# Kernel optimization log

Hardware: AMD Instinct MI355X
Metric: run time of the kernel (lower is better)

## Reference

```python
import jax, jax.numpy as jnp
import numpy as np

N, F_IN, F_OUT = 8192, 256, 256
ALPHA = 0.2  # LeakyReLU negative slope
NEG = -9e15

def setup_inputs() -> dict:
    key = jax.random.key(0)
    k1, k2, k3, k4, k5 = jax.random.split(key, 5)
    h = jax.random.normal(k1, (N, F_IN), dtype=jnp.float32)
    adj = jax.random.randint(k2, (N, N), 0, 2, dtype=jnp.int32)
    W_w = jax.random.normal(k3, (F_IN, F_OUT), dtype=jnp.float32) / np.sqrt(F_IN)
    W_b = jax.random.normal(k4, (F_OUT,), dtype=jnp.float32) * 0.01
    a = jax.random.normal(k5, (2 * F_OUT, 1), dtype=jnp.float32) / np.sqrt(2 * F_OUT)
    return {"h": h, "adj": adj, "W_w": W_w, "W_b": W_b, "a": a}

def reference(h, adj, W_w, W_b, a):
    # Wh: [N, F_OUT]
    Wh = h @ W_w + W_b
    a1 = a[:F_OUT, 0]   # scores for source node i (row)
    a2 = a[F_OUT:, 0]   # scores for target node j (col)
    # e[i,j] = leakyrelu(Wh_i . a1 + Wh_j . a2)  -- separable form of the
    # original repeat/cat construction, identical math without the NxNx2F tensor.
    e = jax.nn.leaky_relu((Wh @ a1)[:, None] + (Wh @ a2)[None, :], negative_slope=ALPHA)
    attention = jnp.where(adj > 0, e, NEG)
    attention = jax.nn.softmax(attention, axis=1)
    # dropout is identity in eval / p=0
    h_prime = attention @ Wh  # [N, F_OUT]
    return h_prime
```

## Files before the change

### kernel.cpp

```cpp
#include <hip/hip_runtime.h>
#include <stdint.h>

#define NN 8192
#define FD 256
#define LOG2E 1.44269504088896340736f
#define SPLIT 8
#define JSLICE (NN / SPLIT)
#define NIT (JSLICE / 32)

typedef __attribute__((ext_vector_type(8))) __bf16 bf16x8;
typedef __attribute__((ext_vector_type(4))) float f32x4;

__device__ __forceinline__ unsigned short f2bf(float x) {
    unsigned u = __float_as_uint(x);
    u = u + 0x7fffu + ((u >> 16) & 1u);
    return (unsigned short)(u >> 16);
}
__device__ __forceinline__ bf16x8 ld_bf8(const unsigned short* p) {
    uint4 v = *(const uint4*)p;
    return __builtin_bit_cast(bf16x8, v);
}
__device__ __forceinline__ unsigned pack_trunc2(float a, float b) {
    return __builtin_amdgcn_perm(__float_as_uint(b), __float_as_uint(a), 0x07060302u);
}
__device__ __forceinline__ void async_ld16(const void* g, void* lds) {
    __builtin_amdgcn_global_load_lds(
        (const __attribute__((address_space(1))) void*)g,
        (__attribute__((address_space(3))) void*)lds, 16, 0, 0);
}

__global__ __launch_bounds__(256) void wtrans_kernel(const float* __restrict__ W,
                                                     unsigned short* __restrict__ WbT) {
    int idx = blockIdx.x * 256 + threadIdx.x;
    int k = idx >> 8, f = idx & 255;
    WbT[f * 256 + k] = f2bf(W[idx]);
}

__global__ __launch_bounds__(256) void gemm1_kernel(const float* __restrict__ h,
                                                    const unsigned short* __restrict__ WbT,
                                                    const float* __restrict__ bias,
                                                    const float* __restrict__ av,
                                                    unsigned short* __restrict__ PBu,
                                                    float* __restrict__ f1p,
                                                    float* __restrict__ f2p) {
    __shared__ float Wh_s[256 * 33];
    __shared__ float red_s[2 * 8 * 32];
    int t = threadIdx.x;
    int l = t & 63, w = t >> 6;
    int jc = (blockIdx.x & 7) * 32 + (blockIdx.x >> 3);
    int i0 = jc * 32;
    int fbase = w * 64;
    int cl = l & 15, q = l >> 4;

    f32x4 acc[2][4] = {};
    const float* hA0 = h + (size_t)(i0 + cl) * FD;
    const float* hA1 = h + (size_t)(i0 + 16 + cl) * FD;

    #pragma unroll
    for (int ks = 0; ks < 8; ++ks) {
        int kk = ks * 32 + q * 8;
        union { unsigned short u[8]; bf16x8 v; } ua0, ua1;
        float4 x0 = *(const float4*)(hA0 + kk);
        float4 x1 = *(const float4*)(hA0 + kk + 4);
        float4 y0 = *(const float4*)(hA1 + kk);
        float4 y1 = *(const float4*)(hA1 + kk + 4);
        ua0.u[0]=f2bf(x0.x); ua0.u[1]=f2bf(x0.y); ua0.u[2]=f2bf(x0.z); ua0.u[3]=f2bf(x0.w);
        ua0.u[4]=f2bf(x1.x); ua0.u[5]=f2bf(x1.y); ua0.u[6]=f2bf(x1.z); ua0.u[7]=f2bf(x1.w);
        ua1.u[0]=f2bf(y0.x); ua1.u[1]=f2bf(y0.y); ua1.u[2]=f2bf(y0.z); ua1.u[3]=f2bf(y0.w);
        ua1.u[4]=f2bf(y1.x); ua1.u[5]=f2bf(y1.y); ua1.u[6]=f2bf(y1.z); ua1.u[7]=f2bf(y1.w);
        #pragma unroll
        for (int bg = 0; bg < 4; ++bg) {
            bf16x8 bF = ld_bf8(WbT + (fbase + bg * 16 + cl) * 256 + kk);
            acc[0][bg] = __builtin_amdgcn_mfma_f32_16x16x32_bf16(ua0.v, bF, acc[0][bg], 0, 0, 0);
            acc[1][bg] = __builtin_amdgcn_mfma_f32_16x16x32_bf16(ua1.v, bF, acc[1][bg], 0, 0, 0);
        }
    }

    #pragma unroll
    for (int mt = 0; mt < 2; ++mt)
        #pragma unroll
        for (int bg = 0; bg < 4; ++bg)
            #pragma unroll
            for (int e = 0; e < 4; ++e) {
                int il = mt * 16 + q * 4 + e;
                int fl = fbase + bg * 16 + cl;
                Wh_s[fl * 33 + il] = acc[mt][bg][e] + bias[fl];
            }
    __syncthreads();
    {
        size_t jcBase = (size_t)jc * 8192;
        #pragma unroll
        for (int u = 0; u < 4; ++u) {
            int fg = u * 4 + (t >> 6);
            int ll = t & 63;
            int c2 = ll & 15, q2 = ll >> 4;
            const float* src = &Wh_s[(fg * 16 + c2) * 33 + q2 * 8];
            union { unsigned short us[8]; uint4 v; } p;
            #pragma unroll
            for (int e = 0; e < 8; ++e) p.us[e] = f2bf(src[e]);
            *(uint4*)(PBu + jcBase + fg * 512 + ll * 8) = p.v;
        }
    }
    {
        int i = t & 31, fc = t >> 5;
        float s1 = 0.f, s2 = 0.f;
        #pragma unroll
        for (int fo = 0; fo < 32; ++fo) {
            int f = fc * 32 + fo;
            float wv = Wh_s[f * 33 + i];
            s1 += wv * av[f];
            s2 += wv * av[256 + f];
        }
        red_s[fc * 32 + i] = s1;
        red_s[256 + fc * 32 + i] = s2;
    }
    __syncthreads();
    if (t < 32) {
        float s = 0.f;
        #pragma unroll
        for (int fc = 0; fc < 8; ++fc) s += red_s[fc * 32 + t];
        f1p[i0 + t] = s * LOG2E;
    } else if (t < 64) {
        int i = t - 32;
        float s = 0.f;
        #pragma unroll
        for (int fc = 0; fc < 8; ++fc) s += red_s[256 + fc * 32 + i];
        f2p[i0 + i] = s * LOG2E;
    }
}

__global__ __launch_bounds__(256, 4) void gat_kernel(const int* __restrict__ adj,
                                                     const unsigned short* __restrict__ PBu,
                                                     const float* __restrict__ f1p,
                                                     const float* __restrict__ f2p,
                                                     float* __restrict__ num,
                                                     float* __restrict__ den) {
    __shared__ __align__(16) unsigned short Bs[2][8192];
    __shared__ unsigned mask_b[2][64];
    __shared__ float f2_s[JSLICE];

    int t = threadIdx.x;
    int l = t & 63, w = t >> 6;
    int s = blockIdx.x & 7;
    int strip = blockIdx.x >> 3;
    int i0b = strip * 64;
    int j0 = s * JSLICE;
    int jw0 = j0 / 32;
    int cl = l & 15, q = l >> 4;

    *(float4*)&f2_s[t * 4] = *(const float4*)(f2p + j0 + t * 4);

    const char* pbBase = (const char*)(PBu + (size_t)jw0 * 8192);
    #pragma unroll
    for (int k = 0; k < 4; ++k)
        async_ld16(pbBase + k * 4096 + t * 16, (char*)&Bs[0][0] + k * 4096 + t * 16);

    const int* arow = adj + (size_t)(i0b + w * 16 + (l >> 5)) * NN + j0 + (l & 31);
    {
        int v0 = arow[0 * 2 * NN], v1 = arow[1 * 2 * NN], v2 = arow[2 * 2 * NN], v3 = arow[3 * 2 * NN];
        int v4 = arow[4 * 2 * NN], v5 = arow[5 * 2 * NN], v6 = arow[6 * 2 * NN], v7 = arow[7 * 2 * NN];
        unsigned long long b0 = __ballot(v0 > 0), b1 = __ballot(v1 > 0);
        unsigned long long b2 = __ballot(v2 > 0), b3 = __ballot(v3 > 0);
        unsigned long long b4 = __ballot(v4 > 0), b5 = __ballot(v5 > 0);
        unsigned long long b6 = __ballot(v6 > 0), b7 = __ballot(v7 > 0);
        if (l == 0) {
            *(uint2*)&mask_b[0][w * 16 + 0]  = make_uint2((unsigned)b0, (unsigned)(b0 >> 32));
            *(uint2*)&mask_b[0][w * 16 + 2]  = make_uint2((unsigned)b1, (unsigned)(b1 >> 32));
            *(uint2*)&mask_b[0][w * 16 + 4]  = make_uint2((unsigned)b2, (unsigned)(b2 >> 32));
            *(uint2*)&mask_b[0][w * 16 + 6]  = make_uint2((unsigned)b3, (unsigned)(b3 >> 32));
            *(uint2*)&mask_b[0][w * 16 + 8]  = make_uint2((unsigned)b4, (unsigned)(b4 >> 32));
            *(uint2*)&mask_b[0][w * 16 + 10] = make_uint2((unsigned)b5, (unsigned)(b5 >> 32));
            *(uint2*)&mask_b[0][w * 16 + 12] = make_uint2((unsigned)b6, (unsigned)(b6 >> 32));
            *(uint2*)&mask_b[0][w * 16 + 14] = make_uint2((unsigned)b7, (unsigned)(b7 >> 32));
        }
    }

    float f1v = f1p[i0b + w * 16 + cl];

    const bf16x8 onesB = __builtin_bit_cast(bf16x8,
        make_uint4(0x3F803F80u, 0x3F803F80u, 0x3F803F80u, 0x3F803F80u));

    f32x4 acc[16] = {};
    f32x4 accR = {};

    #pragma unroll 1
    for (int g = 0; g < NIT; ++g) {
        __syncthreads();
        int a0, a1, a2, a3, a4, a5, a6, a7;
        if (g + 1 < NIT) {
            const char* src = pbBase + (size_t)(g + 1) * 16384;
            char* dst = (char*)&Bs[(g + 1) & 1][0];
            #pragma unroll
            for (int k = 0; k < 4; ++k)
                async_ld16(src + k * 4096 + t * 16, dst + k * 4096 + t * 16);
            int jo = (g + 1) * 32;
            a0 = arow[0 * 2 * NN + jo]; a1 = arow[1 * 2 * NN + jo];
            a2 = arow[2 * 2 * NN + jo]; a3 = arow[3 * 2 * NN + jo];
            a4 = arow[4 * 2 * NN + jo]; a5 = arow[5 * 2 * NN + jo];
            a6 = arow[6 * 2 * NN + jo]; a7 = arow[7 * 2 * NN + jo];
        }

        unsigned mw = mask_b[g & 1][w * 16 + cl];
        float4 F0 = *(const float4*)&f2_s[g * 32 + q * 8];
        float4 F1 = *(const float4*)&f2_s[g * 32 + q * 8 + 4];

        unsigned bits = mw >> (q * 8);
        float fe[8] = {F0.x, F0.y, F0.z, F0.w, F1.x, F1.y, F1.z, F1.w};
        float wv[8];
        #pragma unroll
        for (int e = 0; e < 8; ++e) {
            float sv = f1v + fe[e];
            sv = fmaxf(sv, 0.2f * sv);
            float x = __builtin_amdgcn_exp2f(sv);
            x = (bits >> e) & 1 ? x : 0.f;
            wv[e] = x;
        }
        union { unsigned uu[4]; bf16x8 v; } af;
        af.uu[0] = pack_trunc2(wv[0], wv[1]);
        af.uu[1] = pack_trunc2(wv[2], wv[3]);
        af.uu[2] = pack_trunc2(wv[4], wv[5]);
        af.uu[3] = pack_trunc2(wv[6], wv[7]);

        const unsigned short* bu = &Bs[g & 1][0] + l * 8;
        #pragma unroll
        for (int fg = 0; fg < 16; ++fg) {
            bf16x8 B = ld_bf8(bu + fg * 512);
            acc[fg] = __builtin_amdgcn_mfma_f32_16x16x32_bf16(af.v, B, acc[fg], 0, 0, 0);
        }
        accR = __builtin_amdgcn_mfma_f32_16x16x32_bf16(af.v, onesB, accR, 0, 0, 0);

        if (g + 1 < NIT) {
            int nb = (g + 1) & 1;
            unsigned long long b0 = __ballot(a0 > 0), b1 = __ballot(a1 > 0);
            unsigned long long b2 = __ballot(a2 > 0), b3 = __ballot(a3 > 0);
            unsigned long long b4 = __ballot(a4 > 0), b5 = __ballot(a5 > 0);
            unsigned long long b6 = __ballot(a6 > 0), b7 = __ballot(a7 > 0);
            if (l == 0) {
                *(uint2*)&mask_b[nb][w * 16 + 0]  = make_uint2((unsigned)b0, (unsigned)(b0 >> 32));
                *(uint2*)&mask_b[nb][w * 16 + 2]  = make_uint2((unsigned)b1, (unsigned)(b1 >> 32));
                *(uint2*)&mask_b[nb][w * 16 + 4]  = make_uint2((unsigned)b2, (unsigned)(b2 >> 32));
                *(uint2*)&mask_b[nb][w * 16 + 6]  = make_uint2((unsigned)b3, (unsigned)(b3 >> 32));
                *(uint2*)&mask_b[nb][w * 16 + 8]  = make_uint2((unsigned)b4, (unsigned)(b4 >> 32));
                *(uint2*)&mask_b[nb][w * 16 + 10] = make_uint2((unsigned)b5, (unsigned)(b5 >> 32));
                *(uint2*)&mask_b[nb][w * 16 + 12] = make_uint2((unsigned)b6, (unsigned)(b6 >> 32));
                *(uint2*)&mask_b[nb][w * 16 + 14] = make_uint2((unsigned)b7, (unsigned)(b7 >> 32));
            }
        }
    }

    if (cl == 0) {
        #pragma unroll
        for (int e = 0; e < 4; ++e)
            den[(size_t)s * NN + i0b + w * 16 + q * 4 + e] = accR[e];
    }

    float* nrow = num + (size_t)s * NN * FD;
    #pragma unroll
    for (int e = 0; e < 4; ++e) {
        int r = i0b + w * 16 + q * 4 + e;
        #pragma unroll
        for (int fg = 0; fg < 16; ++fg)
            nrow[(size_t)r * FD + fg * 16 + cl] = acc[fg][e];
    }
}

__global__ __launch_bounds__(256) void combine_kernel(const float* __restrict__ num,
                                                      const float* __restrict__ den,
                                                      float* __restrict__ out) {
    int idx = blockIdx.x * 256 + threadIdx.x;
    int i = idx >> 8;
    float nsum = 0.f, dsum = 0.f;
    #pragma unroll
    for (int s = 0; s < SPLIT; ++s) {
        nsum += num[(size_t)s * NN * FD + idx];
        dsum += den[(size_t)s * NN + i];
    }
    out[idx] = nsum / dsum;
}

extern "C" void kernel_launch(void* const* d_in, const int* in_sizes, int n_in,
                              void* d_out, int out_size, void* d_ws, size_t ws_size,
                              hipStream_t stream) {
    const float* h   = (const float*)d_in[0];
    const int*   adj = (const int*)d_in[1];
    const float* W   = (const float*)d_in[2];
    const float* b   = (const float*)d_in[3];
    const float* a   = (const float*)d_in[4];
    float* out = (float*)d_out;

    char* ws = (char*)d_ws;
    unsigned short* PBu = (unsigned short*)ws;
    unsigned short* WbT = (unsigned short*)(ws + (4u << 20));
    float* f1p = (float*)(ws + (4u << 20) + (128u << 10));
    float* f2p = f1p + NN;
    float* den = f2p + NN;
    float* num = (float*)(ws + (24u << 20));

    wtrans_kernel<<<256, 256, 0, stream>>>(W, WbT);
    gemm1_kernel<<<256, 256, 0, stream>>>(h, WbT, b, a, PBu, f1p, f2p);
    gat_kernel<<<128 * SPLIT, 256, 0, stream>>>(adj, PBu, f1p, f2p, num, den);
    combine_kernel<<<NN * FD / 256, 256, 0, stream>>>(num, den, out);
}
```

Before: 436.1 us.

## Load adjacency as int4 over 64-column chunks with shuffle-built masks

The adjacency read switches from scalar 32-column loads per iteration to 16-byte vector loads covering 64 columns every two iterations. The per-row bitmasks are now built with xor-shuffle OR reductions instead of ballots, and written into a four-slot mask ring. The goal is fewer, wider global load instructions on the dominant adj stream, which is 256 MB of int32, and looser coupling between loads and compute. In exchange the code adds shuffle work, an extra barrier, and more complex slot indexing, which could introduce race or ordering errors.

```diff
diff --git a/kernel.cpp b/kernel.cpp
--- a/kernel.cpp
+++ b/kernel.cpp
@@ -7,6 +7,7 @@
 #define SPLIT 8
 #define JSLICE (NN / SPLIT)
 #define NIT (JSLICE / 32)
+#define NADJ (JSLICE / 64)
 
 typedef __attribute__((ext_vector_type(8))) __bf16 bf16x8;
 typedef __attribute__((ext_vector_type(4))) float f32x4;
@@ -136,7 +137,7 @@
                                                      float* __restrict__ num,
                                                      float* __restrict__ den) {
     __shared__ __align__(16) unsigned short Bs[2][8192];
-    __shared__ unsigned mask_b[2][64];
+    __shared__ unsigned mask_b[4][64];
     __shared__ float f2_s[JSLICE];
 
     int t = threadIdx.x;
@@ -155,27 +156,33 @@
     for (int k = 0; k < 4; ++k)
         async_ld16(pbBase + k * 4096 + t * 16, (char*)&Bs[0][0] + k * 4096 + t * 16);
 
-    const int* arow = adj + (size_t)(i0b + w * 16 + (l >> 5)) * NN + j0 + (l & 31);
+    const int* abase = adj + (size_t)(i0b + w * 16 + (l >> 4)) * NN + j0 + (l & 15) * 4;
+    int4 A0 = *(const int4*)(abase + 0 * 4 * NN);
+    int4 A1 = *(const int4*)(abase + 1 * 4 * NN);
+    int4 A2 = *(const int4*)(abase + 2 * 4 * NN);
+    int4 A3 = *(const int4*)(abase + 3 * 4 * NN);
+
+    float f1v = f1p[i0b + w * 16 + cl];
+
+    __syncthreads();
+
     {
-        int v0 = arow[0 * 2 * NN], v1 = arow[1 * 2 * NN], v2 = arow[2 * 2 * NN], v3 = arow[3 * 2 * NN];
-        int v4 = arow[4 * 2 * NN], v5 = arow[5 * 2 * NN], v6 = arow[6 * 2 * NN], v7 = arow[7 * 2 * NN];
-        unsigned long long b0 = __ballot(v0 > 0), b1 = __ballot(v1 > 0);
-        unsigned long long b2 = __ballot(v2 > 0), b3 = __ballot(v3 > 0);
-        unsigned long long b4 = __ballot(v4 > 0), b5 = __ballot(v5 > 0);
-        unsigned long long b6 = __ballot(v6 > 0), b7 = __ballot(v7 > 0);
-        if (l == 0) {
-            *(uint2*)&mask_b[0][w * 16 + 0]  = make_uint2((unsigned)b0, (unsigned)(b0 >> 32));
-            *(uint2*)&mask_b[0][w * 16 + 2]  = make_uint2((unsigned)b1, (unsigned)(b1 >> 32));
-            *(uint2*)&mask_b[0][w * 16 + 4]  = make_uint2((unsigned)b2, (unsigned)(b2 >> 32));
-            *(uint2*)&mask_b[0][w * 16 + 6]  = make_uint2((unsigned)b3, (unsigned)(b3 >> 32));
-            *(uint2*)&mask_b[0][w * 16 + 8]  = make_uint2((unsigned)b4, (unsigned)(b4 >> 32));
-            *(uint2*)&mask_b[0][w * 16 + 10] = make_uint2((unsigned)b5, (unsigned)(b5 >> 32));
-            *(uint2*)&mask_b[0][w * 16 + 12] = make_uint2((unsigned)b6, (unsigned)(b6 >> 32));
-            *(uint2*)&mask_b[0][w * 16 + 14] = make_uint2((unsigned)b7, (unsigned)(b7 >> 32));
-        }
-    }
-
-    float f1v = f1p[i0b + w * 16 + cl];
+        int word = (l >> 3) & 1;
+        int sh = 4 * (l & 7);
+        int rsub = l >> 4;
+        #pragma unroll
+        for (int ld = 0; ld < 4; ++ld) {
+            int4 A = ld == 0 ? A0 : ld == 1 ? A1 : ld == 2 ? A2 : A3;
+            unsigned n = (unsigned)(A.x > 0) | ((unsigned)(A.y > 0) << 1)
+                       | ((unsigned)(A.z > 0) << 2) | ((unsigned)(A.w > 0) << 3);
+            unsigned v = n << sh;
+            v |= __shfl_xor(v, 1);
+            v |= __shfl_xor(v, 2);
+            v |= __shfl_xor(v, 4);
+            if ((l & 7) == 0)
+                mask_b[word][w * 16 + ld * 4 + rsub] = v;
+        }
+    }
 
     const bf16x8 onesB = __builtin_bit_cast(bf16x8,
         make_uint4(0x3F803F80u, 0x3F803F80u, 0x3F803F80u, 0x3F803F80u));
@@ -186,21 +193,47 @@
     #pragma unroll 1
     for (int g = 0; g < NIT; ++g) {
         __syncthreads();
-        int a0, a1, a2, a3, a4, a5, a6, a7;
+
         if (g + 1 < NIT) {
             const char* src = pbBase + (size_t)(g + 1) * 16384;
             char* dst = (char*)&Bs[(g + 1) & 1][0];
             #pragma unroll
             for (int k = 0; k < 4; ++k)
                 async_ld16(src + k * 4096 + t * 16, dst + k * 4096 + t * 16);
-            int jo = (g + 1) * 32;
-            a0 = arow[0 * 2 * NN + jo]; a1 = arow[1 * 2 * NN + jo];
-            a2 = arow[2 * 2 * NN + jo]; a3 = arow[3 * 2 * NN + jo];
-            a4 = arow[4 * 2 * NN + jo]; a5 = arow[5 * 2 * NN + jo];
-            a6 = arow[6 * 2 * NN + jo]; a7 = arow[7 * 2 * NN + jo];
-        }
-
-        unsigned mw = mask_b[g & 1][w * 16 + cl];
+        }
+
+        if ((g & 1) == 0) {
+            int c1 = g / 2 + 1;
+            if (c1 < NADJ) {
+                int jo = c1 * 64;
+                A0 = *(const int4*)(abase + 0 * 4 * NN + jo);
+                A1 = *(const int4*)(abase + 1 * 4 * NN + jo);
+                A2 = *(const int4*)(abase + 2 * 4 * NN + jo);
+                A3 = *(const int4*)(abase + 3 * 4 * NN + jo);
+            }
+        } else {
+            int c1 = (g + 1) / 2;
+            if (c1 < NADJ) {
+                int word = (l >> 3) & 1;
+                int slot = (g + 1 + word) & 3;
+                int sh = 4 * (l & 7);
+                int rsub = l >> 4;
+                #pragma unroll
+                for (int ld = 0; ld < 4; ++ld) {
+                    int4 A = ld == 0 ? A0 : ld == 1 ? A1 : ld == 2 ? A2 : A3;
+                    unsigned n = (unsigned)(A.x > 0) | ((unsigned)(A.y > 0) << 1)
+                               | ((unsigned)(A.z > 0) << 2) | ((unsigned)(A.w > 0) << 3);
+                    unsigned v = n << sh;
+                    v |= __shfl_xor(v, 1);
+                    v |= __shfl_xor(v, 2);
+                    v |= __shfl_xor(v, 4);
+                    if ((l & 7) == 0)
+                        mask_b[slot][w * 16 + ld * 4 + rsub] = v;
+                }
+            }
+        }
+
+        unsigned mw = mask_b[g & 3][w * 16 + cl];
         float4 F0 = *(const float4*)&f2_s[g * 32 + q * 8];
         float4 F1 = *(const float4*)&f2_s[g * 32 + q * 8 + 4];
 
@@ -228,24 +261,6 @@
             acc[fg] = __builtin_amdgcn_mfma_f32_16x16x32_bf16(af.v, B, acc[fg], 0, 0, 0);
         }
         accR = __builtin_amdgcn_mfma_f32_16x16x32_bf16(af.v, onesB, accR, 0, 0, 0);
-
-        if (g + 1 < NIT) {
-            int nb = (g + 1) & 1;
-            unsigned long long b0 = __ballot(a0 > 0), b1 = __ballot(a1 > 0);
-            unsigned long long b2 = __ballot(a2 > 0), b3 = __ballot(a3 > 0);
-            unsigned long long b4 = __ballot(a4 > 0), b5 = __ballot(a5 > 0);
-            unsigned long long b6 = __ballot(a6 > 0), b7 = __ballot(a7 > 0);
-            if (l == 0) {
-                *(uint2*)&mask_b[nb][w * 16 + 0]  = make_uint2((unsigned)b0, (unsigned)(b0 >> 32));
-                *(uint2*)&mask_b[nb][w * 16 + 2]  = make_uint2((unsigned)b1, (unsigned)(b1 >> 32));
-                *(uint2*)&mask_b[nb][w * 16 + 4]  = make_uint2((unsigned)b2, (unsigned)(b2 >> 32));
-                *(uint2*)&mask_b[nb][w * 16 + 6]  = make_uint2((unsigned)b3, (unsigned)(b3 >> 32));
-                *(uint2*)&mask_b[nb][w * 16 + 8]  = make_uint2((unsigned)b4, (unsigned)(b4 >> 32));
-                *(uint2*)&mask_b[nb][w * 16 + 10] = make_uint2((unsigned)b5, (unsigned)(b5 >> 32));
-                *(uint2*)&mask_b[nb][w * 16 + 12] = make_uint2((unsigned)b6, (unsigned)(b6 >> 32));
-                *(uint2*)&mask_b[nb][w * 16 + 14] = make_uint2((unsigned)b7, (unsigned)(b7 >> 32));
-            }
-        }
     }
 
     if (cl == 0) {
```

New measurement: 428.8 us. About the same (-1.7%).
